# Performance work log

Hardware: AMD Instinct MI355X
Metric: run time of the kernel (lower is better)

## Reference

```python
import jax, jax.numpy as jnp
import numpy as np

B, C, H, W = 2, 256, 48, 48
NH = 8
HD = C // NH  # 32
T = H * W    # 2304


def setup_inputs() -> dict:
    keys = jax.random.split(jax.random.key(0), 16)
    s = lambda fan: 1.0 / np.sqrt(fan)
    x = jax.random.normal(keys[0], (B, C, H, W), jnp.float32)
    wq = jax.random.normal(keys[1], (C, C), jnp.float32) * s(C)
    bq = jax.random.normal(keys[2], (C,), jnp.float32) * 0.01
    wk = jax.random.normal(keys[3], (C, C), jnp.float32) * s(C)
    bk = jax.random.normal(keys[4], (C,), jnp.float32) * 0.01
    wv = jax.random.normal(keys[5], (C, C), jnp.float32) * s(C)
    bv = jax.random.normal(keys[6], (C,), jnp.float32) * 0.01
    wo = jax.random.normal(keys[7], (C, C), jnp.float32) * s(C)
    bo = jax.random.normal(keys[8], (C,), jnp.float32) * 0.01
    gamma1 = jnp.ones((C,), jnp.float32)
    beta1 = jnp.zeros((C,), jnp.float32)
    w1 = jax.random.normal(keys[9], (4 * C, C), jnp.float32) * s(C)
    bf1 = jax.random.normal(keys[10], (4 * C,), jnp.float32) * 0.01
    w2 = jax.random.normal(keys[11], (C, 4 * C), jnp.float32) * s(4 * C)
    bf2 = jax.random.normal(keys[12], (C,), jnp.float32) * 0.01
    gamma2 = jnp.ones((C,), jnp.float32)
    beta2 = jnp.zeros((C,), jnp.float32)
    return dict(x=x, wq=wq, bq=bq, wk=wk, bk=bk, wv=wv, bv=bv, wo=wo, bo=bo,
                gamma1=gamma1, beta1=beta1, w1=w1, bf1=bf1, w2=w2, bf2=bf2,
                gamma2=gamma2, beta2=beta2)


def group_norm1(x, gamma, beta, eps=1e-5):
    # GroupNorm(1, C): normalize over (C, H, W) per sample, per-channel affine.
    mu = jnp.mean(x, axis=(1, 2, 3), keepdims=True)
    var = jnp.mean((x - mu) ** 2, axis=(1, 2, 3), keepdims=True)
    xn = (x - mu) * jax.lax.rsqrt(var + eps)
    return xn * gamma[None, :, None, None] + beta[None, :, None, None]


def reference(x, wq, bq, wk, bk, wv, bv, wo, bo, gamma1, beta1,
              w1, bf1, w2, bf2, gamma2, beta2):
    b, c, h, w = x.shape
    t = h * w
    xt = x.reshape(b, c, t).transpose(0, 2, 1)  # [b, t, c]
    # 1x1 conv == per-token linear
    def heads(y):
        return y.reshape(b, t, NH, HD).transpose(0, 2, 1, 3)  # [b, nh, t, hd]
    q = heads(xt @ wq.T + bq)
    k = heads(xt @ wk.T + bk)
    v = heads(xt @ wv.T + bv)
    # flash SDPA runs in fp16 with fp32 accumulation
    q16 = q.astype(jnp.float16)
    k16 = k.astype(jnp.float16)
    v16 = v.astype(jnp.float16)
    scale = 1.0 / np.sqrt(HD)
    scores = jnp.einsum('bhqd,bhkd->bhqk', q16.astype(jnp.float32),
                        k16.astype(jnp.float32)) * scale
    attn = jax.nn.softmax(scores, axis=-1)
    out = jnp.einsum('bhqk,bhkd->bhqd', attn,
                     v16.astype(jnp.float32)).astype(jnp.float16)
    # remove component along normalized v (fp16, like torch code)
    vn = v16 / jnp.maximum(
        jnp.sqrt(jnp.sum(v16 * v16, axis=-1, keepdims=True)),
        jnp.float16(1e-12))
    out = out - jnp.sum(out * vn, axis=-1, keepdims=True) * vn
    out = out.astype(x.dtype)
    out = out.transpose(0, 2, 1, 3).reshape(b, t, c)  # [b, t, c]
    out = out @ wo.T + bo
    out = out.transpose(0, 2, 1).reshape(b, c, h, w)
    x1 = group_norm1(x + out, gamma1, beta1)
    # FFN: 1x1 conv -> relu -> 1x1 conv, per token
    x1t = x1.reshape(b, c, t).transpose(0, 2, 1)  # [b, t, c]
    hdn = jax.nn.relu(x1t @ w1.T + bf1)
    ffn = (hdn @ w2.T + bf2).transpose(0, 2, 1).reshape(b, c, h, w)
    x2 = group_norm1(x1 + ffn, gamma2, beta2)
    return x2
```

## Files before the change

kernel.cpp:

```cpp
#include <hip/hip_runtime.h>
#include <hip/hip_fp16.h>

typedef _Float16 f16x8 __attribute__((ext_vector_type(8)));
typedef float f32x4 __attribute__((ext_vector_type(4)));

namespace {

constexpr int B = 2, C = 256, T = 2304, F = 1024, NH = 8, HD = 32;
constexpr int BH = B * NH;
constexpr int NCHUNK = 4;
constexpr int CHUNK = T / NCHUNK;
constexpr float SCALE = 0.17677669529663687f;
constexpr float C2 = 0.17677669529663687f * 1.4426950408889634f;
constexpr float INV_N = 1.0f / (float)(C * T);

constexpr size_t N_WQKV = (size_t)3 * C * C;
constexpr size_t N_WO   = (size_t)C * C;
constexpr size_t N_W1   = (size_t)F * C;
constexpr size_t N_W2   = (size_t)C * F;
constexpr size_t N_WALL = N_WQKV + N_WO + N_W1 + N_W2;

constexpr size_t OFF_QKV  = 0;
constexpr size_t SZ_QKV   = (size_t)B * 3 * C * T * 2;
constexpr size_t OFF_AO   = OFF_QKV + SZ_QKV;
constexpr size_t SZ_AO    = (size_t)B * C * T * 2;
constexpr size_t OFF_X1   = OFF_AO + SZ_AO;
constexpr size_t SZ_X1    = (size_t)B * C * T * 4;
constexpr size_t OFF_PART = OFF_X1 + SZ_X1;
constexpr size_t SZ_OP    = (size_t)NCHUNK * BH * HD * T * 2;
constexpr size_t SZ_MP    = (size_t)NCHUNK * BH * T * 4;
constexpr size_t OFF_OP   = OFF_PART;
constexpr size_t OFF_MP   = OFF_OP + SZ_OP;
constexpr size_t OFF_LP   = OFF_MP + SZ_MP;
constexpr size_t SZ_H16   = (size_t)B * F * T * 2;
constexpr size_t SZ_PART  = SZ_OP + 2 * SZ_MP;
constexpr size_t SZ_UNION = SZ_PART > SZ_H16 ? SZ_PART : SZ_H16;
constexpr size_t OFF_H16  = OFF_PART;
constexpr size_t OFF_W16  = OFF_PART + SZ_UNION;
constexpr size_t OFF_BQKV = OFF_W16 + N_WALL * 2;
constexpr size_t OFF_STATS = OFF_BQKV + (size_t)3 * C * 4;

}

__global__ __launch_bounds__(256)
void convert_weights(const float* __restrict__ wq, const float* __restrict__ wk,
                     const float* __restrict__ wv, const float* __restrict__ wo,
                     const float* __restrict__ w1, const float* __restrict__ w2,
                     const float* __restrict__ bq, const float* __restrict__ bk,
                     const float* __restrict__ bv,
                     _Float16* __restrict__ w16, float* __restrict__ bqkv,
                     float* __restrict__ stats)
{
  const size_t tid = (size_t)blockIdx.x * 256 + threadIdx.x;
  if (tid < 8) stats[tid] = 0.f;
  if (tid < 3 * C)
    bqkv[tid] = tid < C ? bq[tid] : (tid < 2 * C ? bk[tid - C] : bv[tid - 2 * C]);
  for (size_t i = tid; i < N_WALL; i += (size_t)gridDim.x * 256) {
    float v;
    if      (i < 65536)  v = wq[i];
    else if (i < 131072) v = wk[i - 65536];
    else if (i < 196608) v = wv[i - 131072];
    else if (i < 262144) v = wo[i - 196608];
    else if (i < 524288) v = w1[i - 262144];
    else                 v = w2[i - 524288];
    w16[i] = (_Float16)v;
  }
}

template<bool RELU, bool RES, bool GNIN, bool GNRES, bool STATS,
         typename InT, typename OutT>
__global__ __launch_bounds__(256)
void gemm_mfma(const _Float16* __restrict__ W, const InT* __restrict__ X,
               const float* __restrict__ bias, const float* __restrict__ res,
               OutT* __restrict__ out, int CO, int K,
               const float* __restrict__ stats_in,
               const float* __restrict__ gamma, const float* __restrict__ beta,
               float* __restrict__ stats_out)
{
  const int b   = blockIdx.z;
  const int co0 = blockIdx.y * 64;
  const int t0  = blockIdx.x * 64;
  const int tid = threadIdx.x;
  const int wid = tid >> 6, lane = tid & 63;
  const int g = lane >> 4, lo = lane & 15;
  const int wm = wid & 1, wn = wid >> 1;

  __shared__ f16x8 xs[4][64];
  __shared__ float gs[256], bs[256];
  __shared__ float red[8];

  float mu = 0.f, rsig = 0.f;
  if (GNIN || GNRES) {
    const float s1 = stats_in[b * 2], s2 = stats_in[b * 2 + 1];
    mu = s1 * INV_N;
    rsig = rsqrtf(s2 * INV_N - mu * mu + 1e-5f);
  }
  if (GNIN) { gs[tid] = gamma[tid]; bs[tid] = beta[tid]; }

  const f32x4 z4 = {0.f, 0.f, 0.f, 0.f};
  f32x4 acc00 = z4, acc01 = z4, acc10 = z4, acc11 = z4;

  const int st = tid & 63;
  const int kp = tid >> 6;
  const InT* Xp = X + (size_t)b * K * T + t0 + st;
  const _Float16* Wp = W + (size_t)(co0 + wm * 32 + lo) * K + 8 * g;

  __syncthreads();

  for (int k0 = 0; k0 < K; k0 += 32) {
    f16x8 wv_;
#pragma unroll
    for (int j = 0; j < 8; ++j) {
      const int k = k0 + kp * 8 + j;
      float v = (float)Xp[(size_t)k * T];
      if (GNIN) v = (v - mu) * rsig * gs[k] + bs[k];
      wv_[j] = (_Float16)v;
    }
    xs[kp][st] = wv_;
    __syncthreads();
    const f16x8 af0 = *(const f16x8*)(Wp + (size_t)k0);
    const f16x8 af1 = *(const f16x8*)(Wp + (size_t)16 * K + k0);
    const f16x8 bf0 = xs[g][wn * 32 + lo];
    const f16x8 bf1 = xs[g][wn * 32 + 16 + lo];
    acc00 = __builtin_amdgcn_mfma_f32_16x16x32_f16(af0, bf0, acc00, 0, 0, 0);
    acc01 = __builtin_amdgcn_mfma_f32_16x16x32_f16(af0, bf1, acc01, 0, 0, 0);
    acc10 = __builtin_amdgcn_mfma_f32_16x16x32_f16(af1, bf0, acc10, 0, 0, 0);
    acc11 = __builtin_amdgcn_mfma_f32_16x16x32_f16(af1, bf1, acc11, 0, 0, 0);
    __syncthreads();
  }

  float s = 0.f, ss = 0.f;
  const size_t obase = ((size_t)b * CO + co0 + wm * 32) * T + t0 + wn * 32 + lo;
  const float* resb = res + obase;
  OutT* outb = out + obase;
  const f32x4 accs[2][2] = {{acc00, acc01}, {acc10, acc11}};
#pragma unroll
  for (int mi = 0; mi < 2; ++mi) {
#pragma unroll
    for (int r = 0; r < 4; ++r) {
      const int row = mi * 16 + 4 * g + r;
      const int co = co0 + wm * 32 + row;
      const float bi = bias[co];
      float gm = 0.f, bt = 0.f;
      if (GNRES) { gm = gamma[co]; bt = beta[co]; }
#pragma unroll
      for (int ni = 0; ni < 2; ++ni) {
        float v = accs[mi][ni][r] + bi;
        if (RES) {
          float rv = resb[(size_t)row * T + ni * 16];
          if (GNRES) rv = (rv - mu) * rsig * gm + bt;
          v += rv;
        }
        if (RELU) v = fmaxf(v, 0.f);
        outb[(size_t)row * T + ni * 16] = (OutT)v;
        if (STATS) { s += v; ss = fmaf(v, v, ss); }
      }
    }
  }

  if (STATS) {
#pragma unroll
    for (int off = 32; off > 0; off >>= 1) {
      s  += __shfl_down(s, off);
      ss += __shfl_down(ss, off);
    }
    if (lane == 0) { red[wid] = s; red[4 + wid] = ss; }
    __syncthreads();
    if (tid == 0) {
      atomicAdd(&stats_out[b * 2],     red[0] + red[1] + red[2] + red[3]);
      atomicAdd(&stats_out[b * 2 + 1], red[4] + red[5] + red[6] + red[7]);
    }
  }
}

__global__ __launch_bounds__(256)
void attn_mfma(const _Float16* __restrict__ qkv, _Float16* __restrict__ opart,
               float* __restrict__ mpart, float* __restrict__ lpart)
{
  const int tid  = threadIdx.x;
  const int wid  = tid >> 6;
  const int lane = tid & 63;
  const int g    = lane >> 4;
  const int lo   = lane & 15;
  const int chunk = blockIdx.y;
  const int bh   = blockIdx.z;
  const int b    = bh >> 3, h = bh & 7;
  const int tq   = blockIdx.x * 64 + wid * 16 + lo;
  const size_t qb = ((size_t)b * 3 * C + h * HD) * T;
  const size_t kb = qb + (size_t)C * T;
  const size_t vb = qb + (size_t)2 * C * T;

  __shared__ _Float16 kt[64][36];
  __shared__ _Float16 vt[32][72];
  __shared__ _Float16 pl[4][16][72];

  f16x8 qf;
#pragma unroll
  for (int j = 0; j < 8; ++j)
    qf[j] = qkv[qb + (size_t)(8 * g + j) * T + tq];

  const f32x4 zero4 = {0.f, 0.f, 0.f, 0.f};
  f32x4 oa[2] = {zero4, zero4};
  float m = -1e30f, l = 0.f;

  for (int it = 0; it < CHUNK / 64; ++it) {
    const int tk0 = chunk * CHUNK + it * 64;
    __syncthreads();
    {
      const int t = tid & 63;
      const int dp0 = tid >> 6;
#pragma unroll
      for (int dd = 0; dd < 4; ++dd) {
        const int d = (dp0 * 4 + dd) * 2;
        const ushort klo = *(const ushort*)(qkv + kb + (size_t)d * T + tk0 + t);
        const ushort khi = *(const ushort*)(qkv + kb + (size_t)(d + 1) * T + tk0 + t);
        *(uint*)&kt[t][d] = (uint)klo | ((uint)khi << 16);
      }
    }
    {
      const int dv = tid >> 3;
      const int seg = tid & 7;
      *(uint4*)&vt[dv][seg * 8] =
          *(const uint4*)(qkv + vb + (size_t)dv * T + tk0 + seg * 8);
    }
    __syncthreads();

    f32x4 s4[4];
#pragma unroll
    for (int mt = 0; mt < 4; ++mt) {
      union { f16x8 v; uint2 u[2]; } kf;
      const _Float16* kr = &kt[mt * 16 + lo][8 * g];
      kf.u[0] = *(const uint2*)(kr);
      kf.u[1] = *(const uint2*)(kr + 4);
      s4[mt] = __builtin_amdgcn_mfma_f32_16x16x32_f16(kf.v, qf, zero4, 0, 0, 0);
    }
    float p[4][4];
    float rmax = -1e30f;
#pragma unroll
    for (int mt = 0; mt < 4; ++mt)
#pragma unroll
      for (int r = 0; r < 4; ++r) {
        p[mt][r] = s4[mt][r] * C2;
        rmax = fmaxf(rmax, p[mt][r]);
      }
    rmax = fmaxf(rmax, __shfl_xor(rmax, 16));
    rmax = fmaxf(rmax, __shfl_xor(rmax, 32));
    const float mn = fmaxf(m, rmax);
    const float fsc = __builtin_amdgcn_exp2f(m - mn);
    m = mn;
    float psum = 0.f;
#pragma unroll
    for (int mt = 0; mt < 4; ++mt)
#pragma unroll
      for (int r = 0; r < 4; ++r) {
        p[mt][r] = __builtin_amdgcn_exp2f(p[mt][r] - mn);
        psum += p[mt][r];
      }
    psum += __shfl_xor(psum, 16);
    psum += __shfl_xor(psum, 32);
    l = l * fsc + psum;
#pragma unroll
    for (int dt = 0; dt < 2; ++dt)
#pragma unroll
      for (int r = 0; r < 4; ++r) oa[dt][r] *= fsc;

#pragma unroll
    for (int mt = 0; mt < 4; ++mt) {
      union { _Float16 e[4]; uint2 u2; } pw;
#pragma unroll
      for (int r = 0; r < 4; ++r) pw.e[r] = (_Float16)p[mt][r];
      *(uint2*)&pl[wid][lo][16 * mt + 4 * g] = pw.u2;
    }
#pragma unroll
    for (int c2 = 0; c2 < 2; ++c2) {
      const f16x8 pbv = *(const f16x8*)&pl[wid][lo][c2 * 32 + 8 * g];
#pragma unroll
      for (int dt = 0; dt < 2; ++dt) {
        const f16x8 vf = *(const f16x8*)&vt[dt * 16 + lo][c2 * 32 + 8 * g];
        oa[dt] = __builtin_amdgcn_mfma_f32_16x16x32_f16(vf, pbv, oa[dt], 0, 0, 0);
      }
    }
  }

  const float invL = 1.f / l;
  const size_t ob = (size_t)(chunk * BH + bh) * HD * T;
#pragma unroll
  for (int dt = 0; dt < 2; ++dt)
#pragma unroll
    for (int r = 0; r < 4; ++r)
      opart[ob + (size_t)(dt * 16 + 4 * g + r) * T + tq] =
          (_Float16)(oa[dt][r] * invL);
  if (g == 0) {
    const size_t pb = (size_t)(chunk * BH + bh) * T + tq;
    mpart[pb] = m;
    lpart[pb] = l;
  }
}

__global__ __launch_bounds__(64)
void attn_combine(const _Float16* __restrict__ opart, const float* __restrict__ mpart,
                  const float* __restrict__ lpart, const _Float16* __restrict__ qkv,
                  _Float16* __restrict__ AOh)
{
  const int q  = blockIdx.x * 64 + threadIdx.x;
  const int bh = blockIdx.y;
  const int b  = bh >> 3, h = bh & 7;
  float mv[NCHUNK], lv[NCHUNK];
  float M = -1e30f;
#pragma unroll
  for (int c = 0; c < NCHUNK; ++c) {
    const size_t pb = (size_t)(c * BH + bh) * T + q;
    mv[c] = mpart[pb];
    lv[c] = lpart[pb];
    M = fmaxf(M, mv[c]);
  }
  float L = 0.f;
  float wc[NCHUNK];
#pragma unroll
  for (int c = 0; c < NCHUNK; ++c) {
    wc[c] = __builtin_amdgcn_exp2f(mv[c] - M) * lv[c];
    L += wc[c];
  }
  const float inv = 1.f / L;
#pragma unroll
  for (int c = 0; c < NCHUNK; ++c) wc[c] *= inv;

  float o[HD];
#pragma unroll
  for (int d = 0; d < HD; ++d) o[d] = 0.f;
#pragma unroll
  for (int c = 0; c < NCHUNK; ++c) {
    const size_t ob = (size_t)(c * BH + bh) * HD * T + q;
#pragma unroll
    for (int d = 0; d < HD; ++d)
      o[d] = fmaf(wc[c], (float)opart[ob + (size_t)d * T], o[d]);
  }

  const size_t vbase = ((size_t)b * 3 * C + 2 * C + h * HD) * T + q;
  float vv[HD], nrm2 = 0.f;
#pragma unroll
  for (int d = 0; d < HD; ++d) {
    vv[d] = (float)qkv[vbase + (size_t)d * T];
    nrm2 = fmaf(vv[d], vv[d], nrm2);
  }
  const float nrm = fmaxf(sqrtf(nrm2), 1e-12f);
  float dot = 0.f;
  float o16[HD], vn[HD];
#pragma unroll
  for (int d = 0; d < HD; ++d) {
    o16[d] = (float)(_Float16)(o[d]);
    vn[d]  = (float)(_Float16)(vv[d] / nrm);
    dot = fmaf(o16[d], vn[d], dot);
  }
  const size_t ab = ((size_t)b * C + h * HD) * T + q;
#pragma unroll
  for (int d = 0; d < HD; ++d)
    AOh[ab + (size_t)d * T] = (_Float16)(o16[d] - dot * vn[d]);
}

__global__ __launch_bounds__(256)
void gn_norm(const float* __restrict__ Y, const float* __restrict__ stats,
             const float* __restrict__ gamma, const float* __restrict__ beta,
             float* __restrict__ O)
{
  const int i = blockIdx.x * 256 + threadIdx.x;
  const int b = i / (C * T);
  const int c = (i / T) & (C - 1);
  const float mu  = stats[b * 2] * INV_N;
  const float var = stats[b * 2 + 1] * INV_N - mu * mu;
  const float r = rsqrtf(var + 1e-5f);
  O[i] = (Y[i] - mu) * r * gamma[c] + beta[c];
}

extern "C" void kernel_launch(void* const* d_in, const int* in_sizes, int n_in,
                              void* d_out, int out_size, void* d_ws, size_t ws_size,
                              hipStream_t stream)
{
  const float* x      = (const float*)d_in[0];
  const float* wq     = (const float*)d_in[1];
  const float* bq     = (const float*)d_in[2];
  const float* wk     = (const float*)d_in[3];
  const float* bk     = (const float*)d_in[4];
  const float* wv     = (const float*)d_in[5];
  const float* bv     = (const float*)d_in[6];
  const float* wo     = (const float*)d_in[7];
  const float* bo     = (const float*)d_in[8];
  const float* gamma1 = (const float*)d_in[9];
  const float* beta1  = (const float*)d_in[10];
  const float* w1     = (const float*)d_in[11];
  const float* bf1    = (const float*)d_in[12];
  const float* w2     = (const float*)d_in[13];
  const float* bf2    = (const float*)d_in[14];
  const float* gamma2 = (const float*)d_in[15];
  const float* beta2  = (const float*)d_in[16];

  char* ws = (char*)d_ws;
  _Float16* qkv16 = (_Float16*)(ws + OFF_QKV);
  _Float16* ao16  = (_Float16*)(ws + OFF_AO);
  float*    x1    = (float*)(ws + OFF_X1);
  _Float16* opart = (_Float16*)(ws + OFF_OP);
  float*    mpart = (float*)(ws + OFF_MP);
  float*    lpart = (float*)(ws + OFF_LP);
  _Float16* h16   = (_Float16*)(ws + OFF_H16);
  _Float16* w16   = (_Float16*)(ws + OFF_W16);
  float*    bqkv  = (float*)(ws + OFF_BQKV);
  float*    stats = (float*)(ws + OFF_STATS);
  float*    out   = (float*)d_out;

  const _Float16* wqkv16 = w16;
  const _Float16* wo16   = w16 + N_WQKV;
  const _Float16* w116   = w16 + N_WQKV + N_WO;
  const _Float16* w216   = w16 + N_WQKV + N_WO + N_W1;

  const dim3 blk256(256);

  convert_weights<<<768, blk256, 0, stream>>>(wq, wk, wv, wo, w1, w2, bq, bk, bv,
                                              w16, bqkv, stats);

  gemm_mfma<false, false, false, false, false, float, _Float16>
      <<<dim3(36, 12, 2), blk256, 0, stream>>>(
          wqkv16, x, bqkv, nullptr, qkv16, 3 * C, C, nullptr, nullptr, nullptr, nullptr);

  attn_mfma<<<dim3(T / 64, NCHUNK, BH), blk256, 0, stream>>>(qkv16, opart, mpart, lpart);
  attn_combine<<<dim3(T / 64, BH), dim3(64), 0, stream>>>(opart, mpart, lpart, qkv16, ao16);

  gemm_mfma<false, true, false, false, true, _Float16, float>
      <<<dim3(36, 4, 2), blk256, 0, stream>>>(
          wo16, ao16, bo, x, x1, C, C, nullptr, nullptr, nullptr, stats);

  gemm_mfma<true, false, true, false, false, float, _Float16>
      <<<dim3(36, 16, 2), blk256, 0, stream>>>(
          w116, x1, bf1, nullptr, h16, F, C, stats, gamma1, beta1, nullptr);

  gemm_mfma<false, true, false, true, true, _Float16, float>
      <<<dim3(36, 4, 2), blk256, 0, stream>>>(
          w216, h16, bf2, x1, out, C, F, stats, gamma1, beta1, stats + 4);

  gn_norm<<<dim3(4608), blk256, 0, stream>>>(out, stats + 4, gamma2, beta2, out);
}
```

Before: 134.6 us.

## Prefetch next K-slice in GEMM, load V directly to registers, prescale Q

The 1x1-conv GEMM kernel now software-pipelines its loop: the next 32-wide slice of X and W is loaded into registers while the current slice is staged in shared memory and multiplied, so global latency can hide behind the MFMAs. The attention kernel drops the V shared-memory tile and reads V fragments straight from global memory into registers. It also folds the softmax scale times log2(e) into Q once, which removes a per-score multiply. The trade-offs are higher register pressure, uncoalesced per-wave V reads that each wave repeats, and Q rounded to fp16 after scaling, which slightly changes numerics.

Measured after the change: 144.8 us. 7.6% more time.

```diff
diff --git a/kernel.cpp b/kernel.cpp
--- a/kernel.cpp
+++ b/kernel.cpp
@@ -10,7 +10,6 @@
 constexpr int BH = B * NH;
 constexpr int NCHUNK = 4;
 constexpr int CHUNK = T / NCHUNK;
-constexpr float SCALE = 0.17677669529663687f;
 constexpr float C2 = 0.17677669529663687f * 1.4426950408889634f;
 constexpr float INV_N = 1.0f / (float)(C * T);
 
@@ -105,21 +104,32 @@
   const InT* Xp = X + (size_t)b * K * T + t0 + st;
   const _Float16* Wp = W + (size_t)(co0 + wm * 32 + lo) * K + 8 * g;
 
+  float xr[8];
+#pragma unroll
+  for (int j = 0; j < 8; ++j) xr[j] = (float)Xp[(size_t)(kp * 8 + j) * T];
+  f16x8 af0 = *(const f16x8*)(Wp);
+  f16x8 af1 = *(const f16x8*)(Wp + (size_t)16 * K);
+
   __syncthreads();
 
   for (int k0 = 0; k0 < K; k0 += 32) {
     f16x8 wv_;
 #pragma unroll
     for (int j = 0; j < 8; ++j) {
-      const int k = k0 + kp * 8 + j;
-      float v = (float)Xp[(size_t)k * T];
-      if (GNIN) v = (v - mu) * rsig * gs[k] + bs[k];
+      float v = xr[j];
+      if (GNIN) { const int k = k0 + kp * 8 + j; v = (v - mu) * rsig * gs[k] + bs[k]; }
       wv_[j] = (_Float16)v;
     }
     xs[kp][st] = wv_;
+
+    const int k1 = (k0 + 32 < K) ? k0 + 32 : k0;
+    float xr2[8];
+#pragma unroll
+    for (int j = 0; j < 8; ++j) xr2[j] = (float)Xp[(size_t)(k1 + kp * 8 + j) * T];
+    const f16x8 afn0 = *(const f16x8*)(Wp + (size_t)k1);
+    const f16x8 afn1 = *(const f16x8*)(Wp + (size_t)16 * K + k1);
+
     __syncthreads();
-    const f16x8 af0 = *(const f16x8*)(Wp + (size_t)k0);
-    const f16x8 af1 = *(const f16x8*)(Wp + (size_t)16 * K + k0);
     const f16x8 bf0 = xs[g][wn * 32 + lo];
     const f16x8 bf1 = xs[g][wn * 32 + 16 + lo];
     acc00 = __builtin_amdgcn_mfma_f32_16x16x32_f16(af0, bf0, acc00, 0, 0, 0);
@@ -127,6 +137,11 @@
     acc10 = __builtin_amdgcn_mfma_f32_16x16x32_f16(af1, bf0, acc10, 0, 0, 0);
     acc11 = __builtin_amdgcn_mfma_f32_16x16x32_f16(af1, bf1, acc11, 0, 0, 0);
     __syncthreads();
+
+#pragma unroll
+    for (int j = 0; j < 8; ++j) xr[j] = xr2[j];
+    af0 = afn0;
+    af1 = afn1;
   }
 
   float s = 0.f, ss = 0.f;
@@ -191,13 +206,12 @@
   const size_t vb = qb + (size_t)2 * C * T;
 
   __shared__ _Float16 kt[64][36];
-  __shared__ _Float16 vt[32][72];
   __shared__ _Float16 pl[4][16][72];
 
   f16x8 qf;
 #pragma unroll
   for (int j = 0; j < 8; ++j)
-    qf[j] = qkv[qb + (size_t)(8 * g + j) * T + tq];
+    qf[j] = (_Float16)((float)qkv[qb + (size_t)(8 * g + j) * T + tq] * C2);
 
   const f32x4 zero4 = {0.f, 0.f, 0.f, 0.f};
   f32x4 oa[2] = {zero4, zero4};
@@ -217,13 +231,15 @@
         *(uint*)&kt[t][d] = (uint)klo | ((uint)khi << 16);
       }
     }
-    {
-      const int dv = tid >> 3;
-      const int seg = tid & 7;
-      *(uint4*)&vt[dv][seg * 8] =
-          *(const uint4*)(qkv + vb + (size_t)dv * T + tk0 + seg * 8);
-    }
     __syncthreads();
+
+    f16x8 vfr[2][2];
+#pragma unroll
+    for (int c2 = 0; c2 < 2; ++c2)
+#pragma unroll
+      for (int dt = 0; dt < 2; ++dt)
+        vfr[c2][dt] = *(const f16x8*)(qkv + vb + (size_t)(dt * 16 + lo) * T +
+                                      tk0 + c2 * 32 + 8 * g);
 
     f32x4 s4[4];
 #pragma unroll
@@ -234,26 +250,25 @@
       kf.u[1] = *(const uint2*)(kr + 4);
       s4[mt] = __builtin_amdgcn_mfma_f32_16x16x32_f16(kf.v, qf, zero4, 0, 0, 0);
     }
-    float p[4][4];
     float rmax = -1e30f;
 #pragma unroll
-    for (int mt = 0; mt < 4; ++mt)
-#pragma unroll
-      for (int r = 0; r < 4; ++r) {
-        p[mt][r] = s4[mt][r] * C2;
-        rmax = fmaxf(rmax, p[mt][r]);
-      }
+    for (int mt = 0; mt < 4; ++mt) {
+      const float m01 = fmaxf(s4[mt][0], s4[mt][1]);
+      const float m23 = fmaxf(s4[mt][2], s4[mt][3]);
+      rmax = fmaxf(rmax, fmaxf(m01, m23));
+    }
     rmax = fmaxf(rmax, __shfl_xor(rmax, 16));
     rmax = fmaxf(rmax, __shfl_xor(rmax, 32));
     const float mn = fmaxf(m, rmax);
     const float fsc = __builtin_amdgcn_exp2f(m - mn);
     m = mn;
+    float p[4][4];
     float psum = 0.f;
 #pragma unroll
     for (int mt = 0; mt < 4; ++mt)
 #pragma unroll
       for (int r = 0; r < 4; ++r) {
-        p[mt][r] = __builtin_amdgcn_exp2f(p[mt][r] - mn);
+        p[mt][r] = __builtin_amdgcn_exp2f(s4[mt][r] - mn);
         psum += p[mt][r];
       }
     psum += __shfl_xor(psum, 16);
@@ -275,10 +290,8 @@
     for (int c2 = 0; c2 < 2; ++c2) {
       const f16x8 pbv = *(const f16x8*)&pl[wid][lo][c2 * 32 + 8 * g];
 #pragma unroll
-      for (int dt = 0; dt < 2; ++dt) {
-        const f16x8 vf = *(const f16x8*)&vt[dt * 16 + lo][c2 * 32 + 8 * g];
-        oa[dt] = __builtin_amdgcn_mfma_f32_16x16x32_f16(vf, pbv, oa[dt], 0, 0, 0);
-      }
+      for (int dt = 0; dt < 2; ++dt)
+        oa[dt] = __builtin_amdgcn_mfma_f32_16x16x32_f16(vfr[c2][dt], pbv, oa[dt], 0, 0, 0);
     }
   }
 
```

## Double-buffer K/V tiles with register prefetch and fold softmax scale into Q

Applied to the files above, without the earlier changes.

The attention kernel now prefetches the next K/V tile into registers while the current tile is computed, storing into alternating shared-memory buffers. This drops one barrier per iteration and hides global load latency. The softmax scale times log2(e) is folded into Q when it is loaded, which removes the per-score multiply. Pre-scaling Q in fp16 changes rounding a little, and the extra buffers and registers raise LDS and register pressure.

Result: faster. 131.4 us (-2.4%).

```diff
diff --git a/kernel.cpp b/kernel.cpp
--- a/kernel.cpp
+++ b/kernel.cpp
@@ -10,7 +10,6 @@
 constexpr int BH = B * NH;
 constexpr int NCHUNK = 4;
 constexpr int CHUNK = T / NCHUNK;
-constexpr float SCALE = 0.17677669529663687f;
 constexpr float C2 = 0.17677669529663687f * 1.4426950408889634f;
 constexpr float INV_N = 1.0f / (float)(C * T);
 
@@ -190,95 +189,122 @@
   const size_t kb = qb + (size_t)C * T;
   const size_t vb = qb + (size_t)2 * C * T;
 
-  __shared__ _Float16 kt[64][36];
-  __shared__ _Float16 vt[32][72];
+  __shared__ _Float16 kt[2][64][36];
+  __shared__ _Float16 vt[2][32][72];
   __shared__ _Float16 pl[4][16][72];
 
+  const int t   = tid & 63;
+  const int dp0 = tid >> 6;
+  const int dv  = tid >> 3;
+  const int seg = tid & 7;
+
   f16x8 qf;
 #pragma unroll
   for (int j = 0; j < 8; ++j)
-    qf[j] = qkv[qb + (size_t)(8 * g + j) * T + tq];
+    qf[j] = (_Float16)((float)qkv[qb + (size_t)(8 * g + j) * T + tq] * C2);
 
   const f32x4 zero4 = {0.f, 0.f, 0.f, 0.f};
   f32x4 oa[2] = {zero4, zero4};
   float m = -1e30f, l = 0.f;
 
-  for (int it = 0; it < CHUNK / 64; ++it) {
+  constexpr int NIT = CHUNK / 64;
+
+  ushort ka[8];
+  uint4  va;
+  {
+    const int tk0 = chunk * CHUNK;
+#pragma unroll
+    for (int dd = 0; dd < 4; ++dd) {
+      const int d = (dp0 * 4 + dd) * 2;
+      ka[2 * dd]     = *(const ushort*)(qkv + kb + (size_t)d * T + tk0 + t);
+      ka[2 * dd + 1] = *(const ushort*)(qkv + kb + (size_t)(d + 1) * T + tk0 + t);
+    }
+    va = *(const uint4*)(qkv + vb + (size_t)dv * T + tk0 + seg * 8);
+  }
+
+  for (int it = 0; it < NIT; ++it) {
+    const int buf = it & 1;
     const int tk0 = chunk * CHUNK + it * 64;
-    __syncthreads();
+
+#pragma unroll
+    for (int dd = 0; dd < 4; ++dd) {
+      const int d = (dp0 * 4 + dd) * 2;
+      *(uint*)&kt[buf][t][d] = (uint)ka[2 * dd] | ((uint)ka[2 * dd + 1] << 16);
+    }
+    *(uint4*)&vt[buf][dv][seg * 8] = va;
+
     {
-      const int t = tid & 63;
-      const int dp0 = tid >> 6;
+      const int tkn = chunk * CHUNK + (it + 1 < NIT ? it + 1 : it) * 64;
+      ushort ka2[8];
+      uint4  va2;
 #pragma unroll
       for (int dd = 0; dd < 4; ++dd) {
         const int d = (dp0 * 4 + dd) * 2;
-        const ushort klo = *(const ushort*)(qkv + kb + (size_t)d * T + tk0 + t);
-        const ushort khi = *(const ushort*)(qkv + kb + (size_t)(d + 1) * T + tk0 + t);
-        *(uint*)&kt[t][d] = (uint)klo | ((uint)khi << 16);
-      }
-    }
-    {
-      const int dv = tid >> 3;
-      const int seg = tid & 7;
-      *(uint4*)&vt[dv][seg * 8] =
-          *(const uint4*)(qkv + vb + (size_t)dv * T + tk0 + seg * 8);
-    }
-    __syncthreads();
-
-    f32x4 s4[4];
-#pragma unroll
-    for (int mt = 0; mt < 4; ++mt) {
-      union { f16x8 v; uint2 u[2]; } kf;
-      const _Float16* kr = &kt[mt * 16 + lo][8 * g];
-      kf.u[0] = *(const uint2*)(kr);
-      kf.u[1] = *(const uint2*)(kr + 4);
-      s4[mt] = __builtin_amdgcn_mfma_f32_16x16x32_f16(kf.v, qf, zero4, 0, 0, 0);
-    }
-    float p[4][4];
-    float rmax = -1e30f;
-#pragma unroll
-    for (int mt = 0; mt < 4; ++mt)
-#pragma unroll
-      for (int r = 0; r < 4; ++r) {
-        p[mt][r] = s4[mt][r] * C2;
-        rmax = fmaxf(rmax, p[mt][r]);
-      }
-    rmax = fmaxf(rmax, __shfl_xor(rmax, 16));
-    rmax = fmaxf(rmax, __shfl_xor(rmax, 32));
-    const float mn = fmaxf(m, rmax);
-    const float fsc = __builtin_amdgcn_exp2f(m - mn);
-    m = mn;
-    float psum = 0.f;
-#pragma unroll
-    for (int mt = 0; mt < 4; ++mt)
-#pragma unroll
-      for (int r = 0; r < 4; ++r) {
-        p[mt][r] = __builtin_amdgcn_exp2f(p[mt][r] - mn);
-        psum += p[mt][r];
-      }
-    psum += __shfl_xor(psum, 16);
-    psum += __shfl_xor(psum, 32);
-    l = l * fsc + psum;
-#pragma unroll
-    for (int dt = 0; dt < 2; ++dt)
-#pragma unroll
-      for (int r = 0; r < 4; ++r) oa[dt][r] *= fsc;
-
-#pragma unroll
-    for (int mt = 0; mt < 4; ++mt) {
-      union { _Float16 e[4]; uint2 u2; } pw;
-#pragma unroll
-      for (int r = 0; r < 4; ++r) pw.e[r] = (_Float16)p[mt][r];
-      *(uint2*)&pl[wid][lo][16 * mt + 4 * g] = pw.u2;
-    }
-#pragma unroll
-    for (int c2 = 0; c2 < 2; ++c2) {
-      const f16x8 pbv = *(const f16x8*)&pl[wid][lo][c2 * 32 + 8 * g];
-#pragma unroll
-      for (int dt = 0; dt < 2; ++dt) {
-        const f16x8 vf = *(const f16x8*)&vt[dt * 16 + lo][c2 * 32 + 8 * g];
-        oa[dt] = __builtin_amdgcn_mfma_f32_16x16x32_f16(vf, pbv, oa[dt], 0, 0, 0);
-      }
+        ka2[2 * dd]     = *(const ushort*)(qkv + kb + (size_t)d * T + tkn + t);
+        ka2[2 * dd + 1] = *(const ushort*)(qkv + kb + (size_t)(d + 1) * T + tkn + t);
+      }
+      va2 = *(const uint4*)(qkv + vb + (size_t)dv * T + tkn + seg * 8);
+
+      __syncthreads();
+
+      f32x4 s4[4];
+#pragma unroll
+      for (int mt = 0; mt < 4; ++mt) {
+        union { f16x8 v; uint2 u[2]; } kf;
+        const _Float16* kr = &kt[buf][mt * 16 + lo][8 * g];
+        kf.u[0] = *(const uint2*)(kr);
+        kf.u[1] = *(const uint2*)(kr + 4);
+        s4[mt] = __builtin_amdgcn_mfma_f32_16x16x32_f16(kf.v, qf, zero4, 0, 0, 0);
+      }
+      float rmax = -1e30f;
+#pragma unroll
+      for (int mt = 0; mt < 4; ++mt) {
+        const float m01 = fmaxf(s4[mt][0], s4[mt][1]);
+        const float m23 = fmaxf(s4[mt][2], s4[mt][3]);
+        rmax = fmaxf(rmax, fmaxf(m01, m23));
+      }
+      rmax = fmaxf(rmax, __shfl_xor(rmax, 16));
+      rmax = fmaxf(rmax, __shfl_xor(rmax, 32));
+      const float mn = fmaxf(m, rmax);
+      const float fsc = __builtin_amdgcn_exp2f(m - mn);
+      m = mn;
+      float p[4][4];
+      float psum = 0.f;
+#pragma unroll
+      for (int mt = 0; mt < 4; ++mt)
+#pragma unroll
+        for (int r = 0; r < 4; ++r) {
+          p[mt][r] = __builtin_amdgcn_exp2f(s4[mt][r] - mn);
+          psum += p[mt][r];
+        }
+      psum += __shfl_xor(psum, 16);
+      psum += __shfl_xor(psum, 32);
+      l = l * fsc + psum;
+#pragma unroll
+      for (int dt = 0; dt < 2; ++dt)
+#pragma unroll
+        for (int r = 0; r < 4; ++r) oa[dt][r] *= fsc;
+
+#pragma unroll
+      for (int mt = 0; mt < 4; ++mt) {
+        union { _Float16 e[4]; uint2 u2; } pw;
+#pragma unroll
+        for (int r = 0; r < 4; ++r) pw.e[r] = (_Float16)p[mt][r];
+        *(uint2*)&pl[wid][lo][16 * mt + 4 * g] = pw.u2;
+      }
+#pragma unroll
+      for (int c2 = 0; c2 < 2; ++c2) {
+        const f16x8 pbv = *(const f16x8*)&pl[wid][lo][c2 * 32 + 8 * g];
+#pragma unroll
+        for (int dt = 0; dt < 2; ++dt) {
+          const f16x8 vf = *(const f16x8*)&vt[buf][dt * 16 + lo][c2 * 32 + 8 * g];
+          oa[dt] = __builtin_amdgcn_mfma_f32_16x16x32_f16(vf, pbv, oa[dt], 0, 0, 0);
+        }
+      }
+
+#pragma unroll
+      for (int j = 0; j < 8; ++j) ka[j] = ka2[j];
+      va = va2;
     }
   }
 
```
